# Performance work log

Measured on AMD Instinct MI355X. Metric: run time of the kernel, lower is better.

Reference implementation:

```python
import jax, jax.numpy as jnp
import numpy as np


def setup_inputs() -> dict:
    key = jax.random.key(0)
    kx, kb, kc, ka, kd = jax.random.split(key, 5)
    B, L, D, N = 8, 4096, 1024, 128
    x = jax.random.normal(kx, (B, L, D), jnp.float32)
    B_w = jax.random.normal(kb, (N, D), jnp.float32) * 0.01  # nn.Linear(d_model->d_state).weight
    C_w = jax.random.normal(kc, (D, N), jnp.float32)         # nn.Linear(d_state->d_model).weight
    # stable negative log_A (HiPPO init gives -|diag|+0.1 < 0)
    log_A = -jax.random.uniform(ka, (N,), jnp.float32) * 3.0 - 0.1
    D_param = jax.random.normal(kd, (D,), jnp.float32)
    return dict(x=x, B_w=B_w, C_w=C_w, log_A=log_A, D_param=D_param)


def reference(x, B_w, C_w, log_A, D_param):
    # x: (B,L,D); B_w: (N,D); C_w: (D,N); log_A: (N,); D_param: (D,)
    A = jnp.exp(log_A)                                   # (N,) diagonal transition
    x_proj = jnp.einsum('bld,nd->bln', x, B_w)           # B @ x  -> (B,L,N)

    def step(h, u):                                      # h_t = A*h_{t-1} + u_t
        h = A * h + u
        return h, h

    h0 = jnp.zeros((x.shape[0], B_w.shape[0]), x.dtype)  # (B,N)
    _, hs = jax.lax.scan(step, h0, jnp.swapaxes(x_proj, 0, 1))  # hs: (L,B,N)

    y = jnp.einsum('lbn,dn->bld', hs, C_w)               # C @ h -> (B,L,D)
    y = y + x * D_param                                  # skip term D*x

    last = x_proj[:, -1, :]                              # (B,N)
    final_state = jnp.broadcast_to(last.mean(axis=0, keepdims=True), last.shape)
    return y, final_state
```

## Files before the change

### kernel.cpp

```cpp
#include <hip/hip_runtime.h>


typedef _Float16 half8 __attribute__((ext_vector_type(8)));
typedef _Float16 half4 __attribute__((ext_vector_type(4)));
typedef float f32x4 __attribute__((ext_vector_type(4)));

#define BDIM 8
#define LDIM 4096
#define DDIM 1024
#define NDIM 128
#define MTOT (BDIM * LDIM)
#define CHUNK 32
#define NCHUNK (LDIM / CHUNK)
#define TOTCHUNK (BDIM * NCHUNK)

__device__ __forceinline__ void dma16(const void* g, void* l) {
    __builtin_amdgcn_global_load_lds((const __attribute__((address_space(1))) void*)g,
                                     (__attribute__((address_space(3))) void*)l, 16, 0, 0);
}

__global__ __launch_bounds__(256) void prep(const float* __restrict__ x,
                                            const float* __restrict__ Bw,
                                            const float* __restrict__ Cw,
                                            _Float16* __restrict__ Bwh,
                                            _Float16* __restrict__ Cwh,
                                            float* __restrict__ out) {
    const int blk = blockIdx.x;
    const int t = threadIdx.x;
    if (blk < 128) {
        const int n = blk;
        float s = 0.f;
        const float* br = Bw + n * DDIM;
        for (int b = 0; b < BDIM; ++b) {
            const float* xr = x + ((size_t)b * LDIM + (LDIM - 1)) * DDIM;
            for (int k = t; k < DDIM; k += 256)
                s = fmaf(xr[k], br[k], s);
        }
        __shared__ float red[256];
        red[t] = s;
        __syncthreads();
        for (int off = 128; off > 0; off >>= 1) {
            if (t < off) red[t] += red[t + off];
            __syncthreads();
        }
        if (t == 0) {
            float v = red[0] * 0.125f;
            for (int b = 0; b < BDIM; ++b)
                out[(size_t)MTOT * DDIM + b * NDIM + n] = v;
        }
    } else {
        const int base = (blk - 128) * 4096;
#pragma unroll
        for (int j = 0; j < 4; ++j) {
            int e = base + j * 1024 + t * 4;
            const float* src;
            _Float16* dst;
            if (e < 131072) { src = Bw + e; dst = Bwh + e; }
            else            { src = Cw + (e - 131072); dst = Cwh + (e - 131072); }
            float4 v = *reinterpret_cast<const float4*>(src);
            half4 h = { (_Float16)v.x, (_Float16)v.y, (_Float16)v.z, (_Float16)v.w };
            *reinterpret_cast<half4*>(dst) = h;
        }
    }
}

__global__ __launch_bounds__(256, 8) void gemm1(const float* __restrict__ x,
                                                const _Float16* __restrict__ Bwh,
                                                const float* __restrict__ logA,
                                                float* __restrict__ xp,
                                                float* __restrict__ agg) {
    __shared__ _Float16 As[32 * 64];
    __shared__ _Float16 Bs[128 * 64];
    const int t = threadIdx.x;
    const int row0 = blockIdx.x * 32;
    const int wave = t >> 6, lane = t & 63;
    const int wr = (wave >> 1) * 16, wc = (wave & 1) * 64;
    const int lrow = lane & 15, kq = (lane >> 4) * 8;
    const int kc = kq >> 3;

    f32x4 acc[4] = {};

    for (int kk = 0; kk < DDIM; kk += 64) {
#pragma unroll
        for (int inst = 0; inst < 4; ++inst) {
            int s = inst * 256 + t;
            int r = s >> 3;
            int cs = (s & 7) ^ (r & 7);
            dma16(&Bwh[(size_t)r * DDIM + kk + cs * 8], &Bs[(inst * 256 + wave * 64) * 8]);
        }
#pragma unroll
        for (int j = 0; j < 2; ++j) {
            int s = t + 256 * j;
            int r = s >> 4, c4 = s & 15;
            float4 v = *reinterpret_cast<const float4*>(&x[(size_t)(row0 + r) * DDIM + kk + c4 * 4]);
            half4 h = { (_Float16)v.x, (_Float16)v.y, (_Float16)v.z, (_Float16)v.w };
            int pc = (c4 >> 1) ^ (r & 7);
            *reinterpret_cast<half4*>(&As[r * 64 + pc * 8 + (c4 & 1) * 4]) = h;
        }
        __syncthreads();

        const int arow = wr + lrow;
#pragma unroll
        for (int ks = 0; ks < 2; ++ks) {
            half8 af = *reinterpret_cast<const half8*>(&As[arow * 64 + ((ks * 4 + kc) ^ (arow & 7)) * 8]);
            half8 bf[4];
#pragma unroll
            for (int ct = 0; ct < 4; ++ct) {
                int brow = wc + ct * 16 + lrow;
                bf[ct] = *reinterpret_cast<const half8*>(&Bs[brow * 64 + ((ks * 4 + kc) ^ (brow & 7)) * 8]);
            }
#pragma unroll
            for (int ct = 0; ct < 4; ++ct)
                acc[ct] = __builtin_amdgcn_mfma_f32_16x16x32_f16(af, bf[ct], acc[ct], 0, 0, 0);
        }
        __syncthreads();
    }

    float* tb = (float*)Bs;
    const int q4 = (lane >> 4) * 4;
#pragma unroll
    for (int ct = 0; ct < 4; ++ct) {
        int col = wc + ct * 16 + lrow;
#pragma unroll
        for (int i = 0; i < 4; ++i)
            tb[(wr + q4 + i) * NDIM + col] = acc[ct][i];
    }
    __syncthreads();
#pragma unroll
    for (int j = 0; j < 4; ++j) {
        int idx = t + 256 * j;
        int row = idx >> 5, c4 = idx & 31;
        *reinterpret_cast<float4*>(&xp[(size_t)(row0 + row) * NDIM + c4 * 4]) =
            *reinterpret_cast<const float4*>(&tb[row * NDIM + c4 * 4]);
    }
    if (t < 128) {
        const float A = expf(logA[t]);
        float h = 0.f;
#pragma unroll
        for (int j = 0; j < CHUNK; ++j)
            h = fmaf(A, h, tb[j * NDIM + t]);
        agg[(size_t)blockIdx.x * NDIM + t] = h;
    }
}

__global__ void scan_carry(const float* __restrict__ agg, const float* __restrict__ logA,
                           float* __restrict__ hprev) {
    const int idx = blockIdx.x * blockDim.x + threadIdx.x;
    const int b = idx >> 7, n = idx & 127;
    const float Ac = expf((float)CHUNK * logA[n]);
    float c = 0.f;
#pragma unroll 8
    for (int ch = 0; ch < NCHUNK; ++ch) {
        int g = (b * NCHUNK + ch) * NDIM + n;
        hprev[g] = c;
        c = fmaf(Ac, c, agg[g]);
    }
}

__global__ void scan_final(const float* __restrict__ xp, const float* __restrict__ logA,
                           const float* __restrict__ hprev, _Float16* __restrict__ hs) {
    const int chunk = blockIdx.x;
    const int n = threadIdx.x;
    const float A = expf(logA[n]);
    float h = hprev[chunk * NDIM + n];
    const float* u = xp + (size_t)chunk * CHUNK * NDIM + n;
    _Float16* o = hs + (size_t)chunk * CHUNK * NDIM + n;
#pragma unroll
    for (int j = 0; j < CHUNK; ++j) {
        h = fmaf(A, h, u[j * NDIM]);
        o[j * NDIM] = (_Float16)h;
    }
}

__global__ __launch_bounds__(256, 3) void gemm2(const _Float16* __restrict__ hs,
                                                const _Float16* __restrict__ Cwh,
                                                const float* __restrict__ x,
                                                const float* __restrict__ Dp,
                                                float* __restrict__ y) {
    __shared__ __align__(16) char smem[49152];
    _Float16* hsP = (_Float16*)smem;
    float* xS = (float*)(smem + 16384);

    const int t = threadIdx.x;
    const int id = blockIdx.x;
    const int xb = (id & 7) * 64 + ((id >> 3) & 63);
    const int yb = id >> 9;
    const int row0 = xb * 64;
    const int col0 = yb * 128;
    const int wave = t >> 6, lane = t & 63;
    const int wr = wave * 16;
    const int lrow = lane & 15, kq = (lane >> 4) * 8;

#pragma unroll
    for (int inst = 0; inst < 4; ++inst) {
        int s = inst * 256 + t;
        int r = s >> 4, c = s & 15;
        dma16(&hs[(size_t)(row0 + r) * NDIM + ((c ^ (r & 7)) * 8)],
              &hsP[(inst * 256 + wave * 64) * 8]);
    }
#pragma unroll
    for (int inst = 0; inst < 8; ++inst) {
        int slab = wave * 8 + inst;
        int r = slab * 2 + (lane >> 5);
        int c = lane & 31;
        dma16(&x[(size_t)(row0 + r) * DDIM + col0 + c * 4], &xS[slab * 256]);
    }
    __syncthreads();

    const _Float16* cb = Cwh + (size_t)(col0 + lrow) * NDIM + kq;
    const int ar = wr + lrow;

    f32x4 acc[8] = {};
#pragma unroll
    for (int kb = 0; kb < 4; ++kb) {
        int ck = kb * 4 + (kq >> 3);
        half8 af = *reinterpret_cast<const half8*>(&hsP[ar * NDIM + ((ck ^ (ar & 7)) * 8)]);
#pragma unroll
        for (int ct = 0; ct < 8; ++ct) {
            half8 bf = *reinterpret_cast<const half8*>(cb + (size_t)ct * 16 * NDIM + kb * 32);
            acc[ct] = __builtin_amdgcn_mfma_f32_16x16x32_f16(af, bf, acc[ct], 0, 0, 0);
        }
    }

    const int q4 = (lane >> 4) * 4;
    float dp[8];
#pragma unroll
    for (int ct = 0; ct < 8; ++ct) dp[ct] = Dp[col0 + ct * 16 + lrow];
#pragma unroll
    for (int ct = 0; ct < 8; ++ct)
#pragma unroll
        for (int i = 0; i < 4; ++i)
            acc[ct][i] = fmaf(xS[(wr + q4 + i) * NDIM + ct * 16 + lrow], dp[ct], acc[ct][i]);

    __syncthreads();
    float* buf = (float*)smem;
#pragma unroll
    for (int ct = 0; ct < 8; ++ct)
#pragma unroll
        for (int i = 0; i < 4; ++i)
            buf[wave * 2112 + (q4 + i) * 132 + ct * 16 + lrow] = acc[ct][i];
    __syncthreads();
#pragma unroll
    for (int j = 0; j < 8; ++j) {
        int idx = t + 256 * j;
        int row = idx >> 5, c4 = idx & 31;
        float4 v = *reinterpret_cast<const float4*>(
            &buf[(row >> 4) * 2112 + (row & 15) * 132 + c4 * 4]);
        *reinterpret_cast<float4*>(&y[(size_t)(row0 + row) * DDIM + col0 + c4 * 4]) = v;
    }
}

extern "C" void kernel_launch(void* const* d_in, const int* in_sizes, int n_in,
                              void* d_out, int out_size, void* d_ws, size_t ws_size,
                              hipStream_t stream) {
    const float* x    = (const float*)d_in[0];
    const float* Bw   = (const float*)d_in[1];
    const float* Cw   = (const float*)d_in[2];
    const float* logA = (const float*)d_in[3];
    const float* Dp   = (const float*)d_in[4];
    float* out = (float*)d_out;

    char* ws = (char*)d_ws;
    float*    xp    = (float*)   (ws);
    _Float16* hs    = (_Float16*)(ws + 16777216);
    float*    agg   = (float*)   (ws + 25165824);
    float*    hprev = (float*)   (ws + 25690112);
    _Float16* Bwh   = (_Float16*)(ws + 26214400);
    _Float16* Cwh   = (_Float16*)(ws + 26476544);

    prep<<<192, 256, 0, stream>>>(x, Bw, Cw, Bwh, Cwh, out);
    gemm1<<<MTOT / 32, 256, 0, stream>>>(x, Bwh, logA, xp, agg);
    scan_carry<<<8, 128, 0, stream>>>(agg, logA, hprev);
    scan_final<<<TOTCHUNK, 128, 0, stream>>>(xp, logA, hprev, hs);
    gemm2<<<4096, 256, 0, stream>>>(hs, Cwh, x, Dp, out);
}
```

Before: 352.2 us.

## Fuse intra-chunk scan into output GEMM and write y directly from registers

Removes the separate scan_final kernel and the fp16 hs buffer. Each gemm2 block now loads its 64 rows of xp into LDS and recomputes two chunks' scan from hprev into swizzled fp16 LDS before the MFMA loop. This saves a launch and the write and re-read of hs. The cost is that the scan is redone once for each of the 8 column blocks. The epilogue also drops the LDS-staged float4 store and instead reads x and writes y per element straight from the accumulators, which gives less coalesced access.

```diff
diff --git a/kernel.cpp b/kernel.cpp
--- a/kernel.cpp
+++ b/kernel.cpp
@@ -157,29 +157,16 @@
     }
 }
 
-__global__ void scan_final(const float* __restrict__ xp, const float* __restrict__ logA,
-                           const float* __restrict__ hprev, _Float16* __restrict__ hs) {
-    const int chunk = blockIdx.x;
-    const int n = threadIdx.x;
-    const float A = expf(logA[n]);
-    float h = hprev[chunk * NDIM + n];
-    const float* u = xp + (size_t)chunk * CHUNK * NDIM + n;
-    _Float16* o = hs + (size_t)chunk * CHUNK * NDIM + n;
-#pragma unroll
-    for (int j = 0; j < CHUNK; ++j) {
-        h = fmaf(A, h, u[j * NDIM]);
-        o[j * NDIM] = (_Float16)h;
-    }
-}
-
-__global__ __launch_bounds__(256, 3) void gemm2(const _Float16* __restrict__ hs,
-                                                const _Float16* __restrict__ Cwh,
-                                                const float* __restrict__ x,
-                                                const float* __restrict__ Dp,
-                                                float* __restrict__ y) {
+__global__ __launch_bounds__(256, 3) void gemm2f(const float* __restrict__ xp,
+                                                 const float* __restrict__ hprev,
+                                                 const float* __restrict__ logA,
+                                                 const _Float16* __restrict__ Cwh,
+                                                 const float* __restrict__ x,
+                                                 const float* __restrict__ Dp,
+                                                 float* __restrict__ y) {
     __shared__ __align__(16) char smem[49152];
-    _Float16* hsP = (_Float16*)smem;
-    float* xS = (float*)(smem + 16384);
+    float* xpS = (float*)smem;
+    _Float16* hsS = (_Float16*)(smem + 32768);
 
     const int t = threadIdx.x;
     const int id = blockIdx.x;
@@ -192,18 +179,23 @@
     const int lrow = lane & 15, kq = (lane >> 4) * 8;
 
 #pragma unroll
-    for (int inst = 0; inst < 4; ++inst) {
-        int s = inst * 256 + t;
-        int r = s >> 4, c = s & 15;
-        dma16(&hs[(size_t)(row0 + r) * NDIM + ((c ^ (r & 7)) * 8)],
-              &hsP[(inst * 256 + wave * 64) * 8]);
-    }
-#pragma unroll
     for (int inst = 0; inst < 8; ++inst) {
         int slab = wave * 8 + inst;
         int r = slab * 2 + (lane >> 5);
         int c = lane & 31;
-        dma16(&x[(size_t)(row0 + r) * DDIM + col0 + c * 4], &xS[slab * 256]);
+        dma16(&xp[(size_t)(row0 + r) * NDIM + c * 4], &xpS[slab * 256]);
+    }
+    const int n = t & 127, ch = t >> 7;
+    float h = hprev[(size_t)(xb * 2 + ch) * NDIM + n];
+    const float An = expf(logA[n]);
+    __syncthreads();
+
+    const int nc = n >> 3, ne = n & 7;
+#pragma unroll
+    for (int j = 0; j < CHUNK; ++j) {
+        int m = ch * CHUNK + j;
+        h = fmaf(An, h, xpS[m * NDIM + n]);
+        hsS[m * NDIM + ((nc ^ (m & 7)) * 8) + ne] = (_Float16)h;
     }
     __syncthreads();
 
@@ -214,7 +206,7 @@
 #pragma unroll
     for (int kb = 0; kb < 4; ++kb) {
         int ck = kb * 4 + (kq >> 3);
-        half8 af = *reinterpret_cast<const half8*>(&hsP[ar * NDIM + ((ck ^ (ar & 7)) * 8)]);
+        half8 af = *reinterpret_cast<const half8*>(&hsS[ar * NDIM + ((ck ^ (ar & 7)) * 8)]);
 #pragma unroll
         for (int ct = 0; ct < 8; ++ct) {
             half8 bf = *reinterpret_cast<const half8*>(cb + (size_t)ct * 16 * NDIM + kb * 32);
@@ -223,30 +215,15 @@
     }
 
     const int q4 = (lane >> 4) * 4;
-    float dp[8];
-#pragma unroll
-    for (int ct = 0; ct < 8; ++ct) dp[ct] = Dp[col0 + ct * 16 + lrow];
-#pragma unroll
-    for (int ct = 0; ct < 8; ++ct)
-#pragma unroll
-        for (int i = 0; i < 4; ++i)
-            acc[ct][i] = fmaf(xS[(wr + q4 + i) * NDIM + ct * 16 + lrow], dp[ct], acc[ct][i]);
-
-    __syncthreads();
-    float* buf = (float*)smem;
-#pragma unroll
-    for (int ct = 0; ct < 8; ++ct)
-#pragma unroll
-        for (int i = 0; i < 4; ++i)
-            buf[wave * 2112 + (q4 + i) * 132 + ct * 16 + lrow] = acc[ct][i];
-    __syncthreads();
-#pragma unroll
-    for (int j = 0; j < 8; ++j) {
-        int idx = t + 256 * j;
-        int row = idx >> 5, c4 = idx & 31;
-        float4 v = *reinterpret_cast<const float4*>(
-            &buf[(row >> 4) * 2112 + (row & 15) * 132 + c4 * 4]);
-        *reinterpret_cast<float4*>(&y[(size_t)(row0 + row) * DDIM + col0 + c4 * 4]) = v;
+#pragma unroll
+    for (int ct = 0; ct < 8; ++ct) {
+        int col = col0 + ct * 16 + lrow;
+        float dp = Dp[col];
+#pragma unroll
+        for (int i = 0; i < 4; ++i) {
+            size_t g = (size_t)(row0 + wr + q4 + i) * DDIM + col;
+            y[g] = fmaf(x[g], dp, acc[ct][i]);
+        }
     }
 }
 
@@ -262,7 +239,6 @@
 
     char* ws = (char*)d_ws;
     float*    xp    = (float*)   (ws);
-    _Float16* hs    = (_Float16*)(ws + 16777216);
     float*    agg   = (float*)   (ws + 25165824);
     float*    hprev = (float*)   (ws + 25690112);
     _Float16* Bwh   = (_Float16*)(ws + 26214400);
@@ -271,6 +247,5 @@
     prep<<<192, 256, 0, stream>>>(x, Bw, Cw, Bwh, Cwh, out);
     gemm1<<<MTOT / 32, 256, 0, stream>>>(x, Bwh, logA, xp, agg);
     scan_carry<<<8, 128, 0, stream>>>(agg, logA, hprev);
-    scan_final<<<TOTCHUNK, 128, 0, stream>>>(xp, logA, hprev, hs);
-    gemm2<<<4096, 256, 0, stream>>>(hs, Cwh, x, Dp, out);
-}
+    gemm2f<<<4096, 256, 0, stream>>>(xp, hprev, logA, Cwh, x, Dp, out);
+}
```

Result: slower. 367.0 us (+4.2%).
